# Performance work log

Measured on AMD Instinct MI355X. Metric: run time of the kernel, lower is better.

Reference implementation:

```python
import jax, jax.numpy as jnp
import numpy as np

N = 50000      # nodes
E = 800000     # edges
IN_CH = 32
H = 64         # hidden_channels
OUT_CH = 16
L = 4          # num_layers
EPS = 1e-7     # GENConv message eps
LN_EPS = 1e-5


def _lin(key, fan_in, fan_out):
    kw, kb = jax.random.split(key)
    s = 1.0 / np.sqrt(fan_in)
    W = jax.random.uniform(kw, (fan_in, fan_out), jnp.float32, -s, s)
    b = jax.random.uniform(kb, (fan_out,), jnp.float32, -s, s)
    return W, b


def setup_inputs() -> dict:
    key = jax.random.key(0)
    ks = jax.random.split(key, 8)
    x = jax.random.normal(ks[0], (N, IN_CH), jnp.float32)
    edge_index = jax.random.randint(ks[1], (2, E), 0, N, dtype=jnp.int32)
    node_W, node_b = _lin(ks[2], IN_CH, H)
    W1, b1, W2, b2 = [], [], [], []
    for i in range(L):
        w1, bb1 = _lin(jax.random.fold_in(ks[3], i), H, 2 * H)
        w2, bb2 = _lin(jax.random.fold_in(ks[4], i), 2 * H, H)
        W1.append(w1); b1.append(bb1); W2.append(w2); b2.append(bb2)
    inp = {
        "x": x,
        "node_W": node_W, "node_b": node_b,
        "W1": jnp.stack(W1), "b1": jnp.stack(b1),          # [L,H,2H],[L,2H]
        "mlp_ln_g": jnp.ones((L, 2 * H), jnp.float32),      # LayerNorm inside GENConv MLP
        "mlp_ln_b": jnp.zeros((L, 2 * H), jnp.float32),
        "W2": jnp.stack(W2), "b2": jnp.stack(b2),          # [L,2H,H],[L,H]
        "t": jnp.ones((L,), jnp.float32),                   # learnable softmax temperature
        "ln_g": jnp.ones((L, H), jnp.float32),              # DeepGCNLayer LayerNorms
        "ln_b": jnp.zeros((L, H), jnp.float32),
        "edge_index": edge_index,
    }
    gW, gb = _lin(ks[5], H, OUT_CH)
    nW, nb = _lin(ks[6], H, OUT_CH + 1)
    inp.update({"g_W": gW, "g_b": gb, "n_W": nW, "n_b": nb})
    return inp


def _layer_norm(h, g, b):
    mu = h.mean(-1, keepdims=True)
    var = ((h - mu) ** 2).mean(-1, keepdims=True)
    return (h - mu) * jax.lax.rsqrt(var + LN_EPS) * g + b


def _gen_conv(h, src, dst, W1, b1, lg, lb, W2, b2, t):
    # message: relu(x_j) + eps  -> [E, H]
    m = jax.nn.relu(h[src]) + EPS
    # per-destination, per-channel scatter softmax with temperature t
    z = t * m
    zmax = jax.ops.segment_max(z, dst, num_segments=N)
    zmax = jnp.where(jnp.isfinite(zmax), zmax, 0.0)  # empty segments -> -inf
    a = jnp.exp(z - zmax[dst])
    denom = jax.ops.segment_sum(a, dst, num_segments=N)
    agg = jax.ops.segment_sum(m * a, dst, num_segments=N) / jnp.maximum(denom, EPS)
    out = agg + h  # root add
    # MLP [H, 2H, H] with LayerNorm + ReLU between
    u = jax.nn.relu(_layer_norm(out @ W1 + b1, lg, lb))
    return u @ W2 + b2


def reference(x, node_W, node_b, W1, b1, mlp_ln_g, mlp_ln_b, W2, b2, t,
              ln_g, ln_b, g_W, g_b, n_W, n_b, edge_index):
    src, dst = edge_index[0], edge_index[1]
    h = x @ node_W + node_b  # node encoder
    # first layer: conv only
    h = _gen_conv(h, src, dst, W1[0], b1[0], mlp_ln_g[0], mlp_ln_b[0], W2[0], b2[0], t[0])
    # remaining res+ blocks: x + conv(relu(norm(x)))  (dropout identity in eval)
    for i in range(1, L):
        y = jax.nn.relu(_layer_norm(h, ln_g[i], ln_b[i]))
        h = h + _gen_conv(y, src, dst, W1[i], b1[i], mlp_ln_g[i], mlp_ln_b[i], W2[i], b2[i], t[i])
    h = jax.nn.relu(_layer_norm(h, ln_g[0], ln_b[0]))
    g_out = jnp.max(h @ g_W + g_b, axis=0)   # batch=None -> global max over nodes
    n_out = h @ n_W + n_b
    return g_out, n_out
```

## Files before the change

### kernel.cpp

```cpp
#include <hip/hip_runtime.h>

#define NN 50000
#define NE 800000
#define INC 32
#define HH 64
#define H2 128
#define OC 16
#define ON 17
#define NL 4
#define MEPS 1e-7f
#define LNE 1e-5f
#define SCAN_BLOCKS 196
#define NOB ((NN + 63) / 64)

typedef __attribute__((ext_vector_type(8))) short bf16x8;
typedef __attribute__((ext_vector_type(4))) float f32x4;

__device__ __forceinline__ unsigned short f2b(float x) {
    unsigned b = __float_as_uint(x);
    b += 0x7FFFu + ((b >> 16) & 1u);
    return (unsigned short)(b >> 16);
}
__device__ __forceinline__ float b2f(unsigned short u) {
    return __uint_as_float(((unsigned)u) << 16);
}

__global__ __launch_bounds__(256) void k_hist2(const int* __restrict__ dst, int* __restrict__ counts,
                                               int* __restrict__ rank) {
    int e = blockIdx.x * 256 + threadIdx.x;
    if (e < NE) rank[e] = atomicAdd(&counts[dst[e]], 1);
}

__global__ __launch_bounds__(256) void k_scan1(const int* __restrict__ counts,
                                               int* __restrict__ incl, int* __restrict__ bsums) {
    __shared__ int s[256];
    int t = threadIdx.x;
    int i = blockIdx.x * 256 + t;
    int v = (i < NN) ? counts[i] : 0;
    s[t] = v;
    __syncthreads();
    for (int off = 1; off < 256; off <<= 1) {
        int x = (t >= off) ? s[t - off] : 0;
        __syncthreads();
        s[t] += x;
        __syncthreads();
    }
    if (i < NN) incl[i] = s[t];
    if (t == 255) bsums[blockIdx.x] = s[255];
}

__global__ __launch_bounds__(256) void k_scan2(int* __restrict__ bsums) {
    __shared__ int s[256];
    int t = threadIdx.x;
    int v = (t < SCAN_BLOCKS) ? bsums[t] : 0;
    s[t] = v;
    __syncthreads();
    for (int off = 1; off < 256; off <<= 1) {
        int x = (t >= off) ? s[t - off] : 0;
        __syncthreads();
        s[t] += x;
        __syncthreads();
    }
    if (t < SCAN_BLOCKS) bsums[t] = s[t] - v;
}

__global__ __launch_bounds__(256) void k_scan3(const int* __restrict__ counts,
                                               int* __restrict__ rowst, const int* __restrict__ bsums) {
    int i = blockIdx.x * 256 + threadIdx.x;
    if (i < NN) rowst[i] = rowst[i] - counts[i] + bsums[blockIdx.x];
}

__global__ __launch_bounds__(256) void k_scatter2(const int* __restrict__ src, const int* __restrict__ dst,
                                                  const int* __restrict__ rank, const int* __restrict__ rowst,
                                                  int* __restrict__ ssrc) {
    int e = blockIdx.x * 256 + threadIdx.x;
    if (e < NE) ssrc[rowst[dst[e]] + rank[e]] = src[e];
}

__global__ __launch_bounds__(256) void k_wprep(const float* __restrict__ W1, const float* __restrict__ W2,
                                               const float* __restrict__ nW, const float* __restrict__ gW,
                                               const float* __restrict__ nbp, const float* __restrict__ gb,
                                               unsigned short* __restrict__ w1h, unsigned short* __restrict__ w1l,
                                               unsigned short* __restrict__ w2h, unsigned short* __restrict__ w2l,
                                               unsigned short* __restrict__ whh, unsigned short* __restrict__ whl,
                                               float* __restrict__ bc) {
    int i = blockIdx.x * 256 + threadIdx.x;
    if (i < 48 * 64) {
        int j = i >> 6, k = i & 63;
        float v = 0.f;
        if (j < ON) v = nW[k * ON + j];
        else if (j < 33) v = gW[k * OC + (j - ON)];
        unsigned short hi = f2b(v);
        whh[i] = hi;
        whl[i] = f2b(v - b2f(hi));
    }
    if (i < 48) bc[i] = (i < ON) ? nbp[i] : ((i < 33) ? gb[i - ON] : 0.f);
    if (i >= NL * H2 * HH) return;
    int l = i / (H2 * HH), r = i % (H2 * HH);
    {
        int c = r / HH, k = r % HH;
        float v = W1[(size_t)l * HH * H2 + (size_t)k * H2 + c];
        unsigned short hi = f2b(v);
        w1h[i] = hi;
        w1l[i] = f2b(v - b2f(hi));
    }
    {
        int c = r / H2, k = r % H2;
        float v = W2[(size_t)l * H2 * HH + (size_t)k * HH + c];
        unsigned short hi = f2b(v);
        w2h[i] = hi;
        w2l[i] = f2b(v - b2f(hi));
    }
}

__global__ __launch_bounds__(256) void k_encoder(const float* __restrict__ x, const float* __restrict__ W,
                                                 const float* __restrict__ b, float* __restrict__ h,
                                                 unsigned short* __restrict__ hbf) {
    __shared__ float Ws[INC * HH];
    __shared__ float bs[HH];
    int tid = threadIdx.x;
    for (int i = tid; i < INC * HH; i += 256) Ws[i] = W[i];
    if (tid < HH) bs[tid] = b[tid];
    __syncthreads();
    int wid = tid >> 6, lane = tid & 63;
    int n = blockIdx.x * 4 + wid;
    if (n >= NN) return;
    float v = (lane < INC) ? x[(size_t)n * INC + lane] : 0.f;
    float acc = bs[lane];
    #pragma unroll
    for (int k = 0; k < INC; ++k)
        acc += __shfl(v, k) * Ws[k * HH + lane];
    h[(size_t)n * HH + lane] = acc;
    hbf[(size_t)n * HH + lane] = f2b(acc);
}

__global__ __launch_bounds__(256) void k_agg(const float* __restrict__ y,
                                             const unsigned short* __restrict__ ybf,
                                             const int* __restrict__ rowst,
                                             const int* __restrict__ counts, const int* __restrict__ ssrc,
                                             const float* __restrict__ tp,
                                             unsigned short* __restrict__ agh,
                                             unsigned short* __restrict__ agl) {
    int tid = threadIdx.x;
    int wid = tid >> 6, lane = tid & 63;
    int n = blockIdx.x * 4 + wid;
    if (n >= NN) return;
    float tval = *tp;
    int start = rowst[n];
    int deg = counts[n];
    float Sa = 0.f, Sma = 0.f;
    if (deg > 0 && deg <= 64) {
        int myidx = (lane < deg) ? ssrc[start + lane] : 0;
        int half = lane >> 5;
        int col = lane & 31;
        float Sa0 = 0.f, Sa1 = 0.f, Sm0 = 0.f, Sm1 = 0.f;
        for (int base = 0; base < deg; base += 16) {
            float c0[8], c1[8];
            int eidx[8];
            #pragma unroll
            for (int i = 0; i < 8; ++i) {
                int e = base + 2 * i + half;
                eidx[i] = e;
                int es = (e < deg) ? e : (deg - 1);
                int s = __shfl(myidx, es);
                unsigned v = *(const unsigned*)(ybf + (size_t)s * HH + col * 2);
                c0[i] = b2f((unsigned short)(v & 0xffffu));
                c1[i] = b2f((unsigned short)(v >> 16));
            }
            #pragma unroll
            for (int i = 0; i < 8; ++i) {
                bool ok = eidx[i] < deg;
                float m0 = fmaxf(c0[i], 0.f) + MEPS;
                float m1 = fmaxf(c1[i], 0.f) + MEPS;
                float a0 = ok ? __expf(tval * m0) : 0.f;
                float a1 = ok ? __expf(tval * m1) : 0.f;
                Sa0 += a0; Sm0 += m0 * a0;
                Sa1 += a1; Sm1 += m1 * a1;
            }
        }
        Sa0 += __shfl_xor(Sa0, 32); Sa1 += __shfl_xor(Sa1, 32);
        Sm0 += __shfl_xor(Sm0, 32); Sm1 += __shfl_xor(Sm1, 32);
        int srcl = lane >> 1;
        float saA = __shfl(Sa0, srcl), saB = __shfl(Sa1, srcl);
        float smA = __shfl(Sm0, srcl), smB = __shfl(Sm1, srcl);
        Sa = (lane & 1) ? saB : saA;
        Sma = (lane & 1) ? smB : smA;
    } else if (deg > 64) {
        for (int e = 0; e < deg; ++e) {
            int s = ssrc[start + e];
            float v = b2f(ybf[(size_t)s * HH + lane]);
            float m = fmaxf(v, 0.f) + MEPS;
            float a = __expf(tval * m);
            Sa += a; Sma += m * a;
        }
    }
    float agg = Sma / fmaxf(Sa, MEPS);
    float av = agg + y[(size_t)n * HH + lane];
    unsigned short hi = f2b(av);
    agh[(size_t)n * HH + lane] = hi;
    agl[(size_t)n * HH + lane] = f2b(av - b2f(hi));
}

__global__ __launch_bounds__(256) void k_mlp(
    const unsigned short* __restrict__ agh, const unsigned short* __restrict__ agl,
    const unsigned short* __restrict__ w1h, const unsigned short* __restrict__ w1l,
    const float* __restrict__ b1,
    const float* __restrict__ mlg, const float* __restrict__ mlb,
    const unsigned short* __restrict__ w2h, const unsigned short* __restrict__ w2l,
    const float* __restrict__ b2,
    const float* __restrict__ hres, float* __restrict__ hout,
    const float* __restrict__ lng1, const float* __restrict__ lnb1,
    float* __restrict__ y, unsigned short* __restrict__ ybf)
{
    __shared__ __align__(16) unsigned short W1hS[128 * 72];
    __shared__ __align__(16) unsigned short W1lS[128 * 72];
    __shared__ __align__(16) unsigned short W2hS[64 * 136];
    __shared__ __align__(16) unsigned short W2lS[64 * 136];
    int tid = threadIdx.x;
    int w = tid >> 6, lane = tid & 63;
    int nl = lane & 15, g = lane >> 4;
    int node = blockIdx.x * 64 + w * 16 + nl;
    bool valid = node < NN;

    bf16x8 bAh[2], bAl[2];
    {
        bf16x8 z = {0, 0, 0, 0, 0, 0, 0, 0};
        if (valid) {
            const unsigned short* rp = agh + (size_t)node * HH + g * 8;
            bAh[0] = *(const bf16x8*)rp;
            bAh[1] = *(const bf16x8*)(rp + 32);
            const unsigned short* rq = agl + (size_t)node * HH + g * 8;
            bAl[0] = *(const bf16x8*)rq;
            bAl[1] = *(const bf16x8*)(rq + 32);
        } else {
            bAh[0] = z; bAh[1] = z; bAl[0] = z; bAl[1] = z;
        }
    }

    #pragma unroll
    for (int it = 0; it < 4; ++it) {
        int c = tid + it * 256;
        int row = c >> 3, col = (c & 7) << 3;
        float4 vh = *(const float4*)(w1h + c * 8);
        float4 vl = *(const float4*)(w1l + c * 8);
        *(float4*)&W1hS[row * 72 + col] = vh;
        *(float4*)&W1lS[row * 72 + col] = vl;
    }
    #pragma unroll
    for (int it = 0; it < 4; ++it) {
        int c = tid + it * 256;
        int row = c >> 4, col = (c & 15) << 3;
        float4 vh = *(const float4*)(w2h + c * 8);
        float4 vl = *(const float4*)(w2l + c * 8);
        *(float4*)&W2hS[row * 136 + col] = vh;
        *(float4*)&W2lS[row * 136 + col] = vl;
    }
    __syncthreads();

    f32x4 accU[8];
    #pragma unroll
    for (int t = 0; t < 8; ++t) {
        int uc = t * 16 + g * 4;
        float4 bb = *(const float4*)(b1 + uc);
        f32x4 a = {bb.x, bb.y, bb.z, bb.w};
        #pragma unroll
        for (int kc = 0; kc < 2; ++kc) {
            int wo = (t * 16 + nl) * 72 + kc * 32 + g * 8;
            bf16x8 ah = *(const bf16x8*)&W1hS[wo];
            bf16x8 al = *(const bf16x8*)&W1lS[wo];
            a = __builtin_amdgcn_mfma_f32_16x16x32_bf16(ah, bAh[kc], a, 0, 0, 0);
            a = __builtin_amdgcn_mfma_f32_16x16x32_bf16(al, bAh[kc], a, 0, 0, 0);
            a = __builtin_amdgcn_mfma_f32_16x16x32_bf16(ah, bAl[kc], a, 0, 0, 0);
        }
        accU[t] = a;
    }

    float s = 0.f, sq = 0.f;
    #pragma unroll
    for (int t = 0; t < 8; ++t) {
        #pragma unroll
        for (int j = 0; j < 4; ++j) { float v = accU[t][j]; s += v; sq += v * v; }
    }
    s += __shfl_xor(s, 16); sq += __shfl_xor(sq, 16);
    s += __shfl_xor(s, 32); sq += __shfl_xor(sq, 32);
    float mu = s * (1.f / 128.f);
    float var = sq * (1.f / 128.f) - mu * mu;
    float rs = rsqrtf(fmaxf(var, 0.f) + LNE);

    __syncthreads();
    unsigned short* myUt = W1hS + w * (16 * 136);

    #pragma unroll
    for (int t = 0; t < 8; ++t) {
        int uc = t * 16 + g * 4;
        float4 gg = *(const float4*)(mlg + uc);
        float4 bb = *(const float4*)(mlb + uc);
        ushort4 pk;
        pk.x = f2b(fmaxf((accU[t][0] - mu) * rs * gg.x + bb.x, 0.f));
        pk.y = f2b(fmaxf((accU[t][1] - mu) * rs * gg.y + bb.y, 0.f));
        pk.z = f2b(fmaxf((accU[t][2] - mu) * rs * gg.z + bb.z, 0.f));
        pk.w = f2b(fmaxf((accU[t][3] - mu) * rs * gg.w + bb.w, 0.f));
        *(ushort4*)(&myUt[nl * 136 + uc]) = pk;
    }
    asm volatile("s_waitcnt lgkmcnt(0)" ::: "memory");

    bf16x8 bB[4];
    #pragma unroll
    for (int kc = 0; kc < 4; ++kc)
        bB[kc] = *(const bf16x8*)(&myUt[nl * 136 + kc * 32 + g * 8]);

    f32x4 accO[4];
    #pragma unroll
    for (int ot = 0; ot < 4; ++ot) {
        int oc = ot * 16 + g * 4;
        float4 bb = *(const float4*)(b2 + oc);
        f32x4 a = {bb.x, bb.y, bb.z, bb.w};
        #pragma unroll
        for (int kc = 0; kc < 4; ++kc) {
            int wo = (ot * 16 + nl) * 136 + kc * 32 + g * 8;
            bf16x8 ah = *(const bf16x8*)&W2hS[wo];
            bf16x8 al = *(const bf16x8*)&W2lS[wo];
            a = __builtin_amdgcn_mfma_f32_16x16x32_bf16(ah, bB[kc], a, 0, 0, 0);
            a = __builtin_amdgcn_mfma_f32_16x16x32_bf16(al, bB[kc], a, 0, 0, 0);
        }
        accO[ot] = a;
    }

    float4 oo[4];
    #pragma unroll
    for (int ot = 0; ot < 4; ++ot) {
        int oc = ot * 16 + g * 4;
        float4 o;
        o.x = accO[ot][0]; o.y = accO[ot][1]; o.z = accO[ot][2]; o.w = accO[ot][3];
        if (valid) {
            if (hres) {
                float4 hr = *(const float4*)(hres + (size_t)node * HH + oc);
                o.x += hr.x; o.y += hr.y; o.z += hr.z; o.w += hr.w;
            }
            *(float4*)(hout + (size_t)node * HH + oc) = o;
        }
        oo[ot] = o;
    }
    if (!lng1) return;

    float s2 = 0.f, sq2 = 0.f;
    #pragma unroll
    for (int ot = 0; ot < 4; ++ot) {
        s2 += oo[ot].x + oo[ot].y + oo[ot].z + oo[ot].w;
        sq2 += oo[ot].x * oo[ot].x + oo[ot].y * oo[ot].y
             + oo[ot].z * oo[ot].z + oo[ot].w * oo[ot].w;
    }
    s2 += __shfl_xor(s2, 16); sq2 += __shfl_xor(sq2, 16);
    s2 += __shfl_xor(s2, 32); sq2 += __shfl_xor(sq2, 32);
    float mu2 = s2 * (1.f / 64.f);
    float var2 = sq2 * (1.f / 64.f) - mu2 * mu2;
    float rs2 = rsqrtf(fmaxf(var2, 0.f) + LNE);
    #pragma unroll
    for (int ot = 0; ot < 4; ++ot) {
        int oc = ot * 16 + g * 4;
        float4 gg = *(const float4*)(lng1 + oc);
        float4 bb = *(const float4*)(lnb1 + oc);
        float4 v;
        v.x = fmaxf((oo[ot].x - mu2) * rs2 * gg.x + bb.x, 0.f);
        v.y = fmaxf((oo[ot].y - mu2) * rs2 * gg.y + bb.y, 0.f);
        v.z = fmaxf((oo[ot].z - mu2) * rs2 * gg.z + bb.z, 0.f);
        v.w = fmaxf((oo[ot].w - mu2) * rs2 * gg.w + bb.w, 0.f);
        if (valid) {
            *(float4*)(y + (size_t)node * HH + oc) = v;
            ushort4 p;
            p.x = f2b(v.x); p.y = f2b(v.y); p.z = f2b(v.z); p.w = f2b(v.w);
            *(ushort4*)(ybf + (size_t)node * HH + oc) = p;
        }
    }
}

__global__ __launch_bounds__(256) void k_outg(const float* __restrict__ h,
                                              const float* __restrict__ lng, const float* __restrict__ lnb,
                                              const unsigned short* __restrict__ whh,
                                              const unsigned short* __restrict__ whl,
                                              const float* __restrict__ bc,
                                              float* __restrict__ dout, float* __restrict__ gmax) {
    __shared__ float smax[4][16];
    int tid = threadIdx.x;
    int w = tid >> 6, lane = tid & 63;
    int nl = lane & 15, g = lane >> 4;
    int node = blockIdx.x * 64 + w * 16 + nl;
    bool valid = node < NN;

    float hv[16];
    if (valid) {
        const float* hp = h + (size_t)node * HH;
        float4 a0 = *(const float4*)(hp + g * 8);
        float4 a1 = *(const float4*)(hp + g * 8 + 4);
        float4 a2 = *(const float4*)(hp + 32 + g * 8);
        float4 a3 = *(const float4*)(hp + 32 + g * 8 + 4);
        hv[0] = a0.x; hv[1] = a0.y; hv[2] = a0.z; hv[3] = a0.w;
        hv[4] = a1.x; hv[5] = a1.y; hv[6] = a1.z; hv[7] = a1.w;
        hv[8] = a2.x; hv[9] = a2.y; hv[10] = a2.z; hv[11] = a2.w;
        hv[12] = a3.x; hv[13] = a3.y; hv[14] = a3.z; hv[15] = a3.w;
    } else {
        #pragma unroll
        for (int i = 0; i < 16; ++i) hv[i] = 0.f;
    }

    float s = 0.f, sq = 0.f;
    #pragma unroll
    for (int i = 0; i < 16; ++i) { s += hv[i]; sq += hv[i] * hv[i]; }
    s += __shfl_xor(s, 16); sq += __shfl_xor(sq, 16);
    s += __shfl_xor(s, 32); sq += __shfl_xor(sq, 32);
    float mu = s * (1.f / 64.f);
    float var = sq * (1.f / 64.f) - mu * mu;
    float rs = rsqrtf(fmaxf(var, 0.f) + LNE);

    union { bf16x8 v; unsigned short u[8]; } Bh[2], Bl[2];
    #pragma unroll
    for (int kc = 0; kc < 2; ++kc) {
        int cb = kc * 32 + g * 8;
        float4 g0 = *(const float4*)(lng + cb);
        float4 g1 = *(const float4*)(lng + cb + 4);
        float4 b0 = *(const float4*)(lnb + cb);
        float4 b1v = *(const float4*)(lnb + cb + 4);
        float gv[8] = {g0.x, g0.y, g0.z, g0.w, g1.x, g1.y, g1.z, g1.w};
        float bv[8] = {b0.x, b0.y, b0.z, b0.w, b1v.x, b1v.y, b1v.z, b1v.w};
        #pragma unroll
        for (int e = 0; e < 8; ++e) {
            float v = fmaxf((hv[kc * 8 + e] - mu) * rs * gv[e] + bv[e], 0.f);
            unsigned short hi = f2b(v);
            Bh[kc].u[e] = hi;
            Bl[kc].u[e] = f2b(v - b2f(hi));
        }
    }

    f32x4 acc[3];
    #pragma unroll
    for (int t = 0; t < 3; ++t) {
        int j0 = t * 16 + g * 4;
        float4 bb = *(const float4*)(bc + j0);
        f32x4 a = {bb.x, bb.y, bb.z, bb.w};
        #pragma unroll
        for (int kc = 0; kc < 2; ++kc) {
            size_t wo = (size_t)(t * 16 + nl) * 64 + kc * 32 + g * 8;
            bf16x8 ah = *(const bf16x8*)(whh + wo);
            bf16x8 al = *(const bf16x8*)(whl + wo);
            a = __builtin_amdgcn_mfma_f32_16x16x32_bf16(ah, Bh[kc].v, a, 0, 0, 0);
            a = __builtin_amdgcn_mfma_f32_16x16x32_bf16(al, Bh[kc].v, a, 0, 0, 0);
            a = __builtin_amdgcn_mfma_f32_16x16x32_bf16(ah, Bl[kc].v, a, 0, 0, 0);
        }
        acc[t] = a;
    }

    #pragma unroll
    for (int t = 0; t < 3; ++t) {
        #pragma unroll
        for (int reg = 0; reg < 4; ++reg) {
            int j = t * 16 + g * 4 + reg;
            float val = acc[t][reg];
            if (j < ON) {
                if (valid) dout[OC + (size_t)node * ON + j] = val;
            } else if (j < 33) {
                float gv = valid ? val : -INFINITY;
                #pragma unroll
                for (int m = 1; m < 16; m <<= 1) gv = fmaxf(gv, __shfl_xor(gv, m));
                if (nl == 0) smax[w][j - ON] = gv;
            }
        }
    }
    __syncthreads();
    if (tid < 16) {
        float m = fmaxf(fmaxf(smax[0][tid], smax[1][tid]),
                        fmaxf(smax[2][tid], smax[3][tid]));
        gmax[(size_t)blockIdx.x * 16 + tid] = m;
    }
}

__global__ void k_gdec(const float* __restrict__ gmax, float* __restrict__ dout) {
    int lane = threadIdx.x & 63;
    int ch = lane & 15, grp = lane >> 4;
    float m = -INFINITY;
    for (int b = grp; b < NOB; b += 4) m = fmaxf(m, gmax[(size_t)b * 16 + ch]);
    m = fmaxf(m, __shfl_xor(m, 16));
    m = fmaxf(m, __shfl_xor(m, 32));
    if (lane < 16) dout[ch] = m;
}

extern "C" void kernel_launch(void* const* d_in, const int* in_sizes, int n_in,
                              void* d_out, int out_size, void* d_ws, size_t ws_size,
                              hipStream_t stream) {
    const float* x     = (const float*)d_in[0];
    const float* nodeW = (const float*)d_in[1];
    const float* nodeB = (const float*)d_in[2];
    const float* W1    = (const float*)d_in[3];
    const float* b1    = (const float*)d_in[4];
    const float* mlg   = (const float*)d_in[5];
    const float* mlb   = (const float*)d_in[6];
    const float* W2    = (const float*)d_in[7];
    const float* b2    = (const float*)d_in[8];
    const float* tt    = (const float*)d_in[9];
    const float* lng   = (const float*)d_in[10];
    const float* lnb   = (const float*)d_in[11];
    const int*   ei    = (const int*)d_in[12];
    const float* gW    = (const float*)d_in[13];
    const float* gb    = (const float*)d_in[14];
    const float* nW    = (const float*)d_in[15];
    const float* nbp   = (const float*)d_in[16];
    float* out = (float*)d_out;

    char* ws = (char*)d_ws;
    size_t off = 0;
    auto alloc = [&](size_t bytes) -> void* {
        void* p = ws + off;
        off = (off + bytes + 255) & ~(size_t)255;
        return p;
    };
    int* counts    = (int*)alloc((size_t)NN * 4);
    size_t zero_end = off;
    float* gmax = (float*)alloc((size_t)NOB * 16 * 4);
    int* bsums = (int*)alloc(1024);
    int* rowst = (int*)alloc((size_t)NN * 4);
    int* ssrc  = (int*)alloc((size_t)NE * 4);
    float* h   = (float*)alloc((size_t)NN * HH * 4);
    float* y   = (float*)alloc((size_t)NN * HH * 4);
    unsigned short* agh = (unsigned short*)alloc((size_t)NN * HH * 2);
    unsigned short* agl = (unsigned short*)alloc((size_t)NN * HH * 2);
    unsigned short* ybf = (unsigned short*)alloc((size_t)NN * HH * 2);
    unsigned short* w1h = (unsigned short*)alloc((size_t)NL * H2 * HH * 2);
    unsigned short* w1l = (unsigned short*)alloc((size_t)NL * H2 * HH * 2);
    unsigned short* w2h = (unsigned short*)alloc((size_t)NL * H2 * HH * 2);
    unsigned short* w2l = (unsigned short*)alloc((size_t)NL * H2 * HH * 2);
    unsigned short* whh = (unsigned short*)alloc((size_t)48 * 64 * 2);
    unsigned short* whl = (unsigned short*)alloc((size_t)48 * 64 * 2);
    float* bc = (float*)alloc(48 * 4);
    int* rank = (int*)agh;

    const int* esrc = ei;
    const int* edst = ei + NE;

    hipMemsetAsync(d_ws, 0, zero_end, stream);

    k_wprep<<<(NL * H2 * HH + 255) / 256, 256, 0, stream>>>(W1, W2, nW, gW, nbp, gb,
                                                            w1h, w1l, w2h, w2l, whh, whl, bc);
    k_hist2<<<(NE + 255) / 256, 256, 0, stream>>>(edst, counts, rank);
    k_scan1<<<SCAN_BLOCKS, 256, 0, stream>>>(counts, rowst, bsums);
    k_scan2<<<1, 256, 0, stream>>>(bsums);
    k_scan3<<<SCAN_BLOCKS, 256, 0, stream>>>(counts, rowst, bsums);
    k_scatter2<<<(NE + 255) / 256, 256, 0, stream>>>(esrc, edst, rank, rowst, ssrc);
    k_encoder<<<(NN + 3) / 4, 256, 0, stream>>>(x, nodeW, nodeB, h, ybf);

    for (int l = 0; l < NL; ++l) {
        const float* yin = (l == 0) ? h : y;
        k_agg<<<(NN + 3) / 4, 256, 0, stream>>>(yin, ybf, rowst, counts, ssrc, tt + l, agh, agl);
        const float* ln1g = (l < NL - 1) ? (lng + (size_t)(l + 1) * HH) : nullptr;
        const float* ln1b = (l < NL - 1) ? (lnb + (size_t)(l + 1) * HH) : nullptr;
        k_mlp<<<(NN + 63) / 64, 256, 0, stream>>>(agh, agl,
                                                  w1h + (size_t)l * H2 * HH, w1l + (size_t)l * H2 * HH,
                                                  b1 + (size_t)l * H2,
                                                  mlg + (size_t)l * H2, mlb + (size_t)l * H2,
                                                  w2h + (size_t)l * H2 * HH, w2l + (size_t)l * H2 * HH,
                                                  b2 + (size_t)l * HH,
                                                  (l == 0) ? (const float*)nullptr : h, h,
                                                  ln1g, ln1b, y, ybf);
    }
    k_outg<<<NOB, 256, 0, stream>>>(h, lng, lnb, whh, whl, bc, out, gmax);
    k_gdec<<<1, 64, 0, stream>>>(gmax, out);
}
```

Baseline: 418.0 us.

## Process two nodes per wavefront in aggregation with packed row metadata

The aggregation kernel now assigns each half-wavefront (32 lanes) to one destination node. Each lane handles two channels, and edges are walked serially in windows of 64 loaded indices, replacing the split-edge scheme with its cross-half reductions and the separate slow path for high-degree nodes. Row start and degree are packed into an int2 meta array written by the scan kernel, so one load replaces two. Both halves loop to the larger of the two node degrees, so imbalanced pairs waste lanes. Per-lane latency also grows because each lane now processes all of its node's edges sequentially.

```diff
diff --git a/kernel.cpp b/kernel.cpp
--- a/kernel.cpp
+++ b/kernel.cpp
@@ -65,9 +65,14 @@
 }
 
 __global__ __launch_bounds__(256) void k_scan3(const int* __restrict__ counts,
-                                               int* __restrict__ rowst, const int* __restrict__ bsums) {
+                                               int* __restrict__ rowst, const int* __restrict__ bsums,
+                                               int2* __restrict__ meta) {
     int i = blockIdx.x * 256 + threadIdx.x;
-    if (i < NN) rowst[i] = rowst[i] - counts[i] + bsums[blockIdx.x];
+    if (i < NN) {
+        int st = rowst[i] - counts[i] + bsums[blockIdx.x];
+        rowst[i] = st;
+        meta[i] = make_int2(st, counts[i]);
+    }
 }
 
 __global__ __launch_bounds__(256) void k_scatter2(const int* __restrict__ src, const int* __restrict__ dst,
@@ -136,40 +141,47 @@
 
 __global__ __launch_bounds__(256) void k_agg(const float* __restrict__ y,
                                              const unsigned short* __restrict__ ybf,
-                                             const int* __restrict__ rowst,
-                                             const int* __restrict__ counts, const int* __restrict__ ssrc,
+                                             const int2* __restrict__ meta,
+                                             const int* __restrict__ ssrc,
                                              const float* __restrict__ tp,
                                              unsigned short* __restrict__ agh,
                                              unsigned short* __restrict__ agl) {
     int tid = threadIdx.x;
-    int wid = tid >> 6, lane = tid & 63;
-    int n = blockIdx.x * 4 + wid;
-    if (n >= NN) return;
+    int w = tid >> 6, lane = tid & 63;
+    int half = lane >> 5;
+    int l = lane & 31;
+    int col = l;
+    int n = blockIdx.x * 8 + w * 2 + half;
+    bool valid = n < NN;
     float tval = *tp;
-    int start = rowst[n];
-    int deg = counts[n];
-    float Sa = 0.f, Sma = 0.f;
-    if (deg > 0 && deg <= 64) {
-        int myidx = (lane < deg) ? ssrc[start + lane] : 0;
-        int half = lane >> 5;
-        int col = lane & 31;
-        float Sa0 = 0.f, Sa1 = 0.f, Sm0 = 0.f, Sm1 = 0.f;
-        for (int base = 0; base < deg; base += 16) {
+    int2 m = valid ? meta[n] : make_int2(0, 0);
+    int start = m.x, deg = m.y;
+
+    int dA = __shfl(deg, 0), dB = __shfl(deg, 32);
+    int dmax = max(dA, dB);
+
+    float Sa0 = 0.f, Sm0 = 0.f, Sa1 = 0.f, Sm1 = 0.f;
+    for (int win = 0; win < dmax; win += 64) {
+        int rem = dmax - win;
+        int wcnt = min(64, rem);
+        int idxLo = (win + l < deg) ? ssrc[start + win + l] : 0;
+        int idxHi = (win + 32 + l < deg) ? ssrc[start + win + 32 + l] : 0;
+        for (int e0 = 0; e0 < wcnt; e0 += 8) {
             float c0[8], c1[8];
-            int eidx[8];
+            int ev[8];
             #pragma unroll
             for (int i = 0; i < 8; ++i) {
-                int e = base + 2 * i + half;
-                eidx[i] = e;
-                int es = (e < deg) ? e : (deg - 1);
-                int s = __shfl(myidx, es);
+                int e = e0 + i;
+                ev[i] = win + e;
+                int sel = (e < 32) ? idxLo : idxHi;
+                int s = __shfl(sel, (lane & 32) | (e & 31));
                 unsigned v = *(const unsigned*)(ybf + (size_t)s * HH + col * 2);
                 c0[i] = b2f((unsigned short)(v & 0xffffu));
                 c1[i] = b2f((unsigned short)(v >> 16));
             }
             #pragma unroll
             for (int i = 0; i < 8; ++i) {
-                bool ok = eidx[i] < deg;
+                bool ok = ev[i] < deg;
                 float m0 = fmaxf(c0[i], 0.f) + MEPS;
                 float m1 = fmaxf(c1[i], 0.f) + MEPS;
                 float a0 = ok ? __expf(tval * m0) : 0.f;
@@ -178,27 +190,18 @@
                 Sa1 += a1; Sm1 += m1 * a1;
             }
         }
-        Sa0 += __shfl_xor(Sa0, 32); Sa1 += __shfl_xor(Sa1, 32);
-        Sm0 += __shfl_xor(Sm0, 32); Sm1 += __shfl_xor(Sm1, 32);
-        int srcl = lane >> 1;
-        float saA = __shfl(Sa0, srcl), saB = __shfl(Sa1, srcl);
-        float smA = __shfl(Sm0, srcl), smB = __shfl(Sm1, srcl);
-        Sa = (lane & 1) ? saB : saA;
-        Sma = (lane & 1) ? smB : smA;
-    } else if (deg > 64) {
-        for (int e = 0; e < deg; ++e) {
-            int s = ssrc[start + e];
-            float v = b2f(ybf[(size_t)s * HH + lane]);
-            float m = fmaxf(v, 0.f) + MEPS;
-            float a = __expf(tval * m);
-            Sa += a; Sma += m * a;
-        }
-    }
-    float agg = Sma / fmaxf(Sa, MEPS);
-    float av = agg + y[(size_t)n * HH + lane];
-    unsigned short hi = f2b(av);
-    agh[(size_t)n * HH + lane] = hi;
-    agl[(size_t)n * HH + lane] = f2b(av - b2f(hi));
+    }
+    if (!valid) return;
+    float agg0 = Sm0 / fmaxf(Sa0, MEPS);
+    float agg1 = Sm1 / fmaxf(Sa1, MEPS);
+    float2 yv = *(const float2*)(y + (size_t)n * HH + col * 2);
+    float av0 = agg0 + yv.x;
+    float av1 = agg1 + yv.y;
+    unsigned short h0 = f2b(av0), h1 = f2b(av1);
+    ushort2 ph = {h0, h1};
+    ushort2 pl = {f2b(av0 - b2f(h0)), f2b(av1 - b2f(h1))};
+    *(ushort2*)(agh + (size_t)n * HH + col * 2) = ph;
+    *(ushort2*)(agl + (size_t)n * HH + col * 2) = pl;
 }
 
 __global__ __launch_bounds__(256) void k_mlp(
@@ -517,6 +520,7 @@
     float* gmax = (float*)alloc((size_t)NOB * 16 * 4);
     int* bsums = (int*)alloc(1024);
     int* rowst = (int*)alloc((size_t)NN * 4);
+    int2* meta = (int2*)alloc((size_t)NN * 8);
     int* ssrc  = (int*)alloc((size_t)NE * 4);
     float* h   = (float*)alloc((size_t)NN * HH * 4);
     float* y   = (float*)alloc((size_t)NN * HH * 4);
@@ -542,13 +546,13 @@
     k_hist2<<<(NE + 255) / 256, 256, 0, stream>>>(edst, counts, rank);
     k_scan1<<<SCAN_BLOCKS, 256, 0, stream>>>(counts, rowst, bsums);
     k_scan2<<<1, 256, 0, stream>>>(bsums);
-    k_scan3<<<SCAN_BLOCKS, 256, 0, stream>>>(counts, rowst, bsums);
+    k_scan3<<<SCAN_BLOCKS, 256, 0, stream>>>(counts, rowst, bsums, meta);
     k_scatter2<<<(NE + 255) / 256, 256, 0, stream>>>(esrc, edst, rank, rowst, ssrc);
     k_encoder<<<(NN + 3) / 4, 256, 0, stream>>>(x, nodeW, nodeB, h, ybf);
 
     for (int l = 0; l < NL; ++l) {
         const float* yin = (l == 0) ? h : y;
-        k_agg<<<(NN + 3) / 4, 256, 0, stream>>>(yin, ybf, rowst, counts, ssrc, tt + l, agh, agl);
+        k_agg<<<(NN + 7) / 8, 256, 0, stream>>>(yin, ybf, meta, ssrc, tt + l, agh, agl);
         const float* ln1g = (l < NL - 1) ? (lng + (size_t)(l + 1) * HH) : nullptr;
         const float* ln1b = (l < NL - 1) ? (lnb + (size_t)(l + 1) * HH) : nullptr;
         k_mlp<<<(NN + 63) / 64, 256, 0, stream>>>(agh, agl,
```

New measurement: 407.3 us. -2.6%, faster.
